# Optimization experiments

Measured on AMD Instinct MI355X. Metric: run time of the kernel, lower is better.

The kernel has to match this reference:

```python
import jax, jax.numpy as jnp
import numpy as np


def _parse_bounds(valid):
    # valid: (n, R, L) bool, True where label < griding_num.
    # Faithfully replicates the Python loop semantics of the original parser.
    R = valid.shape[1]
    v0 = valid[:, 0, :]            # row 0 valid
    v1 = valid[:, 1, :]            # row 1 valid
    vlast = valid[:, -1, :]        # last row valid
    # top: 0 if row0 valid, else first invalid->valid transition index + 1
    up = (~valid[:, :-1, :]) & valid[:, 1:, :]          # (n, R-1, L)
    has_up = jnp.any(up, axis=1)
    first_up = jnp.argmax(up, axis=1) + 1
    top = jnp.where(v0, 0, jnp.where(has_up, first_up, 0))
    top_exists = v0 | has_up
    # down: per loop order -> if (row0 valid & row1 invalid): 0 (break at j=0)
    #       elif last row valid: R-1 (fires at j=0 before any later transition)
    #       else first valid->invalid transition index
    dn = valid[:, :-1, :] & (~valid[:, 1:, :])           # (n, R-1, L)
    has_dn = jnp.any(dn, axis=1)
    first_dn = jnp.argmax(dn, axis=1)
    cond0 = v0 & (~v1)
    down = jnp.where(cond0, 0, jnp.where(vlast, R - 1, jnp.where(has_dn, first_dn, 0)))
    down_exists = cond0 | vlast | has_dn
    exists = top_exists & down_exists
    top = jnp.where(exists, top, 0)
    down = jnp.where(exists, down, 0)
    return top, down  # each (n, L) int


def _forward(x, labels):
    n, dim, R, L = x.shape
    g = dim - 1  # griding_num
    probs = jax.nn.softmax(x[:, :g, :, :], axis=1)               # (n, g, R, L)
    emb = jnp.arange(g, dtype=x.dtype).reshape(1, g, 1, 1)
    pos = jnp.sum(probs * emb, axis=1)                           # (n, R, L) expected grid position

    valid = labels < g                                           # (n, R, L)
    top, down = _parse_bounds(valid)                             # (n, L)

    # first differences along rows, then |second differences|
    d = pos[:, :-1, :] - pos[:, 1:, :]                           # (n, R-1, L)
    sec = jnp.abs(d[:, :-1, :] - d[:, 1:, :])                    # (n, R-2, L)

    idx = jnp.arange(R - 2).reshape(1, R - 2, 1)
    top_b = top[:, None, :]
    down_b = down[:, None, :]
    mask = (idx >= top_b) & (idx <= down_b - 2)                  # second-diff indices i in [top, down-2]

    count = down - top - 1                                       # = len(diff_list1) - 1
    lane_sum = jnp.sum(sec * mask.astype(x.dtype), axis=1)       # (n, L)
    lane_loss = lane_sum / jnp.maximum(count, 1).astype(x.dtype)
    lane_loss = jnp.where(count >= 1, lane_loss, jnp.zeros_like(lane_loss))

    NUM_LANES_IN_LOSS = 4
    loss_k = jnp.sum(lane_loss[:, :NUM_LANES_IN_LOSS], axis=1) / 8.0  # (n,)
    flag = jnp.sum(loss_k != 0)
    total = jnp.sum(loss_k)
    return jnp.where(flag > 0, total / flag.astype(x.dtype), jnp.zeros((), dtype=x.dtype))


def setup_inputs() -> dict:
    key = jax.random.key(0)
    k1, k2 = jax.random.split(key)
    x = jax.random.normal(k1, (4096, 101, 56, 4), dtype=jnp.float32)
    labels = jax.random.randint(k2, (4096, 56, 4), 0, 101).astype(jnp.int64)
    return {"x": x, "labels": labels}


def reference(x, labels):
    return _forward(x, labels)
```

## Files before the change

### kernel.cpp

```cpp
#include <hip/hip_runtime.h>

#define G   100
#define DIM 101
#define R   56
#define L   4
#define RL  224
#define NBLK 1024

__global__ __launch_bounds__(256) void pos_loss_kernel(
    const float* __restrict__ x, const int* __restrict__ labels,
    float2* __restrict__ partials)
{
    __shared__ float pos_s[4 * RL];
    __shared__ float lane_loss_s[16];
    __shared__ float blk_red[8];

    const int t     = threadIdx.x;
    const int n_sub = t >> 6;
    const int q     = t & 63;
    const long long n = (long long)blockIdx.x * 4 + n_sub;

    if (q < 56) {
        const float* xp = x + (size_t)n * DIM * RL + 4 * q;
        float s0 = 0.f, s1 = 0.f, s2 = 0.f, s3 = 0.f;
        float w0 = 0.f, w1 = 0.f, w2 = 0.f, w3 = 0.f;
        #pragma unroll 4
        for (int c = 0; c < G; ++c) {
            float4 v = *(const float4*)(xp + (size_t)c * RL);
            float fc = (float)c;
            float e0 = __expf(v.x);
            float e1 = __expf(v.y);
            float e2 = __expf(v.z);
            float e3 = __expf(v.w);
            s0 += e0; s1 += e1; s2 += e2; s3 += e3;
            w0 = fmaf(fc, e0, w0);
            w1 = fmaf(fc, e1, w1);
            w2 = fmaf(fc, e2, w2);
            w3 = fmaf(fc, e3, w3);
        }
        float* ps = pos_s + n_sub * RL + 4 * q;
        ps[0] = w0 / s0;
        ps[1] = w1 / s1;
        ps[2] = w2 / s2;
        ps[3] = w3 / s3;
    }
    __syncthreads();

    if (t < 16) {
        const int ns = t >> 2;
        const int l  = t & 3;
        const long long nn = (long long)blockIdx.x * 4 + ns;
        const int* lp = labels + (size_t)nn * RL + l;

        unsigned long long m = 0ull;
        #pragma unroll
        for (int r = 0; r < R; ++r)
            m |= (unsigned long long)(lp[r * 4] < G) << r;

        const unsigned long long MASK55 = (1ull << 55) - 1ull;
        const bool v0    = (m & 1ull) != 0;
        const bool v1    = (m & 2ull) != 0;
        const bool vlast = ((m >> (R - 1)) & 1ull) != 0;

        unsigned long long up = (~m) & (m >> 1) & MASK55;
        unsigned long long dn = m & (~(m >> 1)) & MASK55;
        const bool has_up = (up != 0ull);
        const bool has_dn = (dn != 0ull);
        const int first_up = has_up ? (__builtin_ctzll(up) + 1) : 0;
        const int first_dn = has_dn ? __builtin_ctzll(dn) : 0;

        int  top        = v0 ? 0 : (has_up ? first_up : 0);
        const bool top_exists = v0 || has_up;
        const bool cond0 = v0 && !v1;
        int  down       = cond0 ? 0 : (vlast ? (R - 1) : (has_dn ? first_dn : 0));
        const bool down_exists = cond0 || vlast || has_dn;
        if (!(top_exists && down_exists)) { top = 0; down = 0; }

        const int count = down - top - 1;
        float lane_loss = 0.f;
        if (count >= 1) {
            const float* pr = pos_s + ns * RL + l;
            float sum = 0.f;
            const int hi = down - 2;
            for (int idx = top; idx <= hi; ++idx) {
                float p0 = pr[4 * idx];
                float p1 = pr[4 * (idx + 1)];
                float p2 = pr[4 * (idx + 2)];
                sum += fabsf(p0 - 2.f * p1 + p2);
            }
            lane_loss = sum / (float)count;
        }
        lane_loss_s[t] = lane_loss;
    }
    __syncthreads();

    if (t < 4) {
        float lk = (lane_loss_s[t * 4 + 0] + lane_loss_s[t * 4 + 1] +
                    lane_loss_s[t * 4 + 2] + lane_loss_s[t * 4 + 3]) * 0.125f;
        blk_red[t]     = lk;
        blk_red[t + 4] = (lk != 0.0f) ? 1.f : 0.f;
    }
    __syncthreads();

    if (t == 0) {
        float2 p;
        p.x = blk_red[0] + blk_red[1] + blk_red[2] + blk_red[3];
        p.y = blk_red[4] + blk_red[5] + blk_red[6] + blk_red[7];
        partials[blockIdx.x] = p;
    }
}

__global__ __launch_bounds__(256) void reduce_kernel(
    const float2* __restrict__ partials, float* __restrict__ out)
{
    __shared__ float sred[4], cred[4];
    const int t = threadIdx.x;
    float s = 0.f, c = 0.f;
    #pragma unroll
    for (int i = 0; i < NBLK / 256; ++i) {
        float2 p = partials[t + i * 256];
        s += p.x;
        c += p.y;
    }
    #pragma unroll
    for (int off = 32; off >= 1; off >>= 1) {
        s += __shfl_down(s, off, 64);
        c += __shfl_down(c, off, 64);
    }
    if ((t & 63) == 0) { sred[t >> 6] = s; cred[t >> 6] = c; }
    __syncthreads();
    if (t == 0) {
        float tot = sred[0] + sred[1] + sred[2] + sred[3];
        float f   = cred[0] + cred[1] + cred[2] + cred[3];
        out[0] = (f > 0.f) ? (tot / f) : 0.0f;
    }
}

extern "C" void kernel_launch(void* const* d_in, const int* in_sizes, int n_in,
                              void* d_out, int out_size, void* d_ws, size_t ws_size,
                              hipStream_t stream) {
    const float* x      = (const float*)d_in[0];
    const int*   labels = (const int*)d_in[1];
    float*       out    = (float*)d_out;
    float2*      partials = (float2*)d_ws;

    const int N = in_sizes[1] / RL;
    pos_loss_kernel<<<N / 4, 256, 0, stream>>>(x, labels, partials);
    reduce_kernel<<<1, 256, 0, stream>>>(partials, out);
}
```

Measured before the change: 488.2 us.

## Split channel reduction across two waves per sample and use wave-level bound parsing

Each block now handles one sample with two waves, each summing half of the 100 channels, and the partial sums are combined through shared memory. Validity masks are built with wave ballots, and the second differences and masked sums use shuffles instead of a serial loop in a few threads. Loads of x use non-temporal hints. This should raise memory-level parallelism and cut the serial tail work, at the cost of four times as many blocks and a larger partials buffer.

```diff
diff --git a/kernel.cpp b/kernel.cpp
--- a/kernel.cpp
+++ b/kernel.cpp
@@ -5,29 +5,52 @@
 #define R   56
 #define L   4
 #define RL  224
-#define NBLK 1024
+#define NS  4096
 
-__global__ __launch_bounds__(256) void pos_loss_kernel(
+typedef float floatx4 __attribute__((ext_vector_type(4)));
+
+struct Bounds { int top, down, count; };
+
+__device__ __forceinline__ Bounds parse_bounds(unsigned long long m) {
+    const unsigned long long MASK55 = (1ull << 55) - 1ull;
+    const bool v0    = (m & 1ull) != 0;
+    const bool v1    = (m & 2ull) != 0;
+    const bool vlast = ((m >> (R - 1)) & 1ull) != 0;
+    unsigned long long up = (~m) & (m >> 1) & MASK55;
+    unsigned long long dn = m & (~(m >> 1)) & MASK55;
+    const bool has_up = (up != 0ull);
+    const bool has_dn = (dn != 0ull);
+    const int first_up = has_up ? (__builtin_ctzll(up) + 1) : 0;
+    const int first_dn = has_dn ? __builtin_ctzll(dn) : 0;
+    int top = v0 ? 0 : (has_up ? first_up : 0);
+    const bool top_exists = v0 || has_up;
+    const bool cond0 = v0 && !v1;
+    int down = cond0 ? 0 : (vlast ? (R - 1) : (has_dn ? first_dn : 0));
+    const bool down_exists = cond0 || vlast || has_dn;
+    if (!(top_exists && down_exists)) { top = 0; down = 0; }
+    Bounds b; b.top = top; b.down = down; b.count = down - top - 1;
+    return b;
+}
+
+__global__ __launch_bounds__(128) void pos_loss_kernel(
     const float* __restrict__ x, const int* __restrict__ labels,
     float2* __restrict__ partials)
 {
-    __shared__ float pos_s[4 * RL];
-    __shared__ float lane_loss_s[16];
-    __shared__ float blk_red[8];
+    __shared__ float comb[8][R];
 
-    const int t     = threadIdx.x;
-    const int n_sub = t >> 6;
-    const int q     = t & 63;
-    const long long n = (long long)blockIdx.x * 4 + n_sub;
+    const int t    = threadIdx.x;
+    const int wave = t >> 6;
+    const int q    = t & 63;
+    const int n    = blockIdx.x;
 
+    float s0 = 0.f, s1 = 0.f, s2 = 0.f, s3 = 0.f;
+    float w0 = 0.f, w1 = 0.f, w2 = 0.f, w3 = 0.f;
     if (q < 56) {
-        const float* xp = x + (size_t)n * DIM * RL + 4 * q;
-        float s0 = 0.f, s1 = 0.f, s2 = 0.f, s3 = 0.f;
-        float w0 = 0.f, w1 = 0.f, w2 = 0.f, w3 = 0.f;
-        #pragma unroll 4
-        for (int c = 0; c < G; ++c) {
-            float4 v = *(const float4*)(xp + (size_t)c * RL);
-            float fc = (float)c;
+        const float* xp = x + (size_t)n * (DIM * RL) + (size_t)(wave * 50) * RL + 4 * q;
+        #pragma unroll 5
+        for (int c = 0; c < 50; ++c) {
+            floatx4 v = __builtin_nontemporal_load((const floatx4*)(xp + (size_t)c * RL));
+            float fc = (float)(c + wave * 50);
             float e0 = __expf(v.x);
             float e1 = __expf(v.y);
             float e2 = __expf(v.z);
@@ -38,75 +61,66 @@
             w2 = fmaf(fc, e2, w2);
             w3 = fmaf(fc, e3, w3);
         }
-        float* ps = pos_s + n_sub * RL + 4 * q;
-        ps[0] = w0 / s0;
-        ps[1] = w1 / s1;
-        ps[2] = w2 / s2;
-        ps[3] = w3 / s3;
+    }
+
+    if (wave == 1 && q < 56) {
+        comb[0][q] = s0; comb[1][q] = s1; comb[2][q] = s2; comb[3][q] = s3;
+        comb[4][q] = w0; comb[5][q] = w1; comb[6][q] = w2; comb[7][q] = w3;
     }
     __syncthreads();
 
-    if (t < 16) {
-        const int ns = t >> 2;
-        const int l  = t & 3;
-        const long long nn = (long long)blockIdx.x * 4 + ns;
-        const int* lp = labels + (size_t)nn * RL + l;
+    if (wave != 0) return;
 
-        unsigned long long m = 0ull;
-        #pragma unroll
-        for (int r = 0; r < R; ++r)
-            m |= (unsigned long long)(lp[r * 4] < G) << r;
+    float p0 = 0.f, p1 = 0.f, p2 = 0.f, p3 = 0.f;
+    int4 lab = make_int4(G, G, G, G);
+    if (q < 56) {
+        p0 = (w0 + comb[4][q]) / (s0 + comb[0][q]);
+        p1 = (w1 + comb[5][q]) / (s1 + comb[1][q]);
+        p2 = (w2 + comb[6][q]) / (s2 + comb[2][q]);
+        p3 = (w3 + comb[7][q]) / (s3 + comb[3][q]);
+        lab = *(const int4*)(labels + (size_t)n * RL + 4 * q);
+    }
 
-        const unsigned long long MASK55 = (1ull << 55) - 1ull;
-        const bool v0    = (m & 1ull) != 0;
-        const bool v1    = (m & 2ull) != 0;
-        const bool vlast = ((m >> (R - 1)) & 1ull) != 0;
+    const bool inrow = (q < 56);
+    unsigned long long m0 = __ballot(inrow && (lab.x < G));
+    unsigned long long m1 = __ballot(inrow && (lab.y < G));
+    unsigned long long m2 = __ballot(inrow && (lab.z < G));
+    unsigned long long m3 = __ballot(inrow && (lab.w < G));
 
-        unsigned long long up = (~m) & (m >> 1) & MASK55;
-        unsigned long long dn = m & (~(m >> 1)) & MASK55;
-        const bool has_up = (up != 0ull);
-        const bool has_dn = (dn != 0ull);
-        const int first_up = has_up ? (__builtin_ctzll(up) + 1) : 0;
-        const int first_dn = has_dn ? __builtin_ctzll(dn) : 0;
+    Bounds b0 = parse_bounds(m0);
+    Bounds b1 = parse_bounds(m1);
+    Bounds b2 = parse_bounds(m2);
+    Bounds b3 = parse_bounds(m3);
 
-        int  top        = v0 ? 0 : (has_up ? first_up : 0);
-        const bool top_exists = v0 || has_up;
-        const bool cond0 = v0 && !v1;
-        int  down       = cond0 ? 0 : (vlast ? (R - 1) : (has_dn ? first_dn : 0));
-        const bool down_exists = cond0 || vlast || has_dn;
-        if (!(top_exists && down_exists)) { top = 0; down = 0; }
+    float d0 = p0 - __shfl_down(p0, 1, 64);
+    float d1 = p1 - __shfl_down(p1, 1, 64);
+    float d2 = p2 - __shfl_down(p2, 1, 64);
+    float d3 = p3 - __shfl_down(p3, 1, 64);
+    float e0 = fabsf(d0 - __shfl_down(d0, 1, 64));
+    float e1 = fabsf(d1 - __shfl_down(d1, 1, 64));
+    float e2 = fabsf(d2 - __shfl_down(d2, 1, 64));
+    float e3 = fabsf(d3 - __shfl_down(d3, 1, 64));
 
-        const int count = down - top - 1;
-        float lane_loss = 0.f;
-        if (count >= 1) {
-            const float* pr = pos_s + ns * RL + l;
-            float sum = 0.f;
-            const int hi = down - 2;
-            for (int idx = top; idx <= hi; ++idx) {
-                float p0 = pr[4 * idx];
-                float p1 = pr[4 * (idx + 1)];
-                float p2 = pr[4 * (idx + 2)];
-                sum += fabsf(p0 - 2.f * p1 + p2);
-            }
-            lane_loss = sum / (float)count;
-        }
-        lane_loss_s[t] = lane_loss;
+    float c0 = (q >= b0.top && q <= b0.down - 2) ? e0 : 0.f;
+    float c1 = (q >= b1.top && q <= b1.down - 2) ? e1 : 0.f;
+    float c2 = (q >= b2.top && q <= b2.down - 2) ? e2 : 0.f;
+    float c3 = (q >= b3.top && q <= b3.down - 2) ? e3 : 0.f;
+
+    #pragma unroll
+    for (int off = 32; off >= 1; off >>= 1) {
+        c0 += __shfl_down(c0, off, 64);
+        c1 += __shfl_down(c1, off, 64);
+        c2 += __shfl_down(c2, off, 64);
+        c3 += __shfl_down(c3, off, 64);
     }
-    __syncthreads();
 
-    if (t < 4) {
-        float lk = (lane_loss_s[t * 4 + 0] + lane_loss_s[t * 4 + 1] +
-                    lane_loss_s[t * 4 + 2] + lane_loss_s[t * 4 + 3]) * 0.125f;
-        blk_red[t]     = lk;
-        blk_red[t + 4] = (lk != 0.0f) ? 1.f : 0.f;
-    }
-    __syncthreads();
-
-    if (t == 0) {
-        float2 p;
-        p.x = blk_red[0] + blk_red[1] + blk_red[2] + blk_red[3];
-        p.y = blk_red[4] + blk_red[5] + blk_red[6] + blk_red[7];
-        partials[blockIdx.x] = p;
+    if (q == 0) {
+        float ll0 = c0 / fmaxf((float)b0.count, 1.f);
+        float ll1 = c1 / fmaxf((float)b1.count, 1.f);
+        float ll2 = c2 / fmaxf((float)b2.count, 1.f);
+        float ll3 = c3 / fmaxf((float)b3.count, 1.f);
+        float lk = (ll0 + ll1 + ll2 + ll3) * 0.125f;
+        partials[n] = make_float2(lk, (lk != 0.0f) ? 1.f : 0.f);
     }
 }
 
@@ -117,7 +131,7 @@
     const int t = threadIdx.x;
     float s = 0.f, c = 0.f;
     #pragma unroll
-    for (int i = 0; i < NBLK / 256; ++i) {
+    for (int i = 0; i < NS / 256; ++i) {
         float2 p = partials[t + i * 256];
         s += p.x;
         c += p.y;
@@ -139,12 +153,12 @@
 extern "C" void kernel_launch(void* const* d_in, const int* in_sizes, int n_in,
                               void* d_out, int out_size, void* d_ws, size_t ws_size,
                               hipStream_t stream) {
-    const float* x      = (const float*)d_in[0];
-    const int*   labels = (const int*)d_in[1];
-    float*       out    = (float*)d_out;
+    const float* x        = (const float*)d_in[0];
+    const int*   labels   = (const int*)d_in[1];
+    float*       out      = (float*)d_out;
     float2*      partials = (float2*)d_ws;
 
     const int N = in_sizes[1] / RL;
-    pos_loss_kernel<<<N / 4, 256, 0, stream>>>(x, labels, partials);
+    pos_loss_kernel<<<N, 128, 0, stream>>>(x, labels, partials);
     reduce_kernel<<<1, 256, 0, stream>>>(partials, out);
 }
```

Result: faster. 455.9 us (-6.6%).
